# Kernel tuning notes

Measured on AMD Instinct MI355X. Metric: run time of the kernel, lower is better.

## Reference

```python
import jax, jax.numpy as jnp
import numpy as np

B, S, E, H = 4, 2048, 1024, 16
D = E // H  # head dim = 64

def setup_inputs() -> dict:
    key = jax.random.key(0)
    k1, k2, k3 = jax.random.split(key, 3)
    scale = 0.02
    return {
        "x": jax.random.normal(k1, (B, S, E), dtype=jnp.float32),
        "W_qkv": jax.random.normal(k2, (E, 3 * E), dtype=jnp.float32) * scale,
        "b_qkv": jnp.zeros((3 * E,), dtype=jnp.float32),
        "W_o": jax.random.normal(k3, (E, E), dtype=jnp.float32) * scale,
        "b_o": jnp.zeros((E,), dtype=jnp.float32),
    }

def reference(x, W_qkv, b_qkv, W_o, b_o):
    # dropout is identity in eval mode
    qkv = x @ W_qkv + b_qkv                      # [B, S, 3E]
    q, k, v = jnp.split(qkv, 3, axis=-1)          # each [B, S, E]
    def split_heads(t):
        return t.reshape(B, S, H, D).transpose(0, 2, 1, 3)  # [B, H, S, D]
    q, k, v = split_heads(q), split_heads(k), split_heads(v)
    scores = jnp.einsum("bhsd,bhtd->bhst", q, k) / jnp.sqrt(jnp.float32(D))
    causal = jnp.tril(jnp.ones((S, S), dtype=bool))
    scores = jnp.where(causal[None, None], scores, jnp.float32(-jnp.inf))
    attn = jax.nn.softmax(scores, axis=-1)        # [B, H, S, S]
    out = jnp.einsum("bhst,bhtd->bhsd", attn, v)  # [B, H, S, D]
    out = out.transpose(0, 2, 1, 3).reshape(B, S, E)
    return out @ W_o + b_o
```

## Files before the change

### kernel.cpp

```cpp
#include <hip/hip_runtime.h>
#include <stdint.h>

typedef __bf16 bf16_t;
typedef __bf16 bf16x8 __attribute__((ext_vector_type(8)));
typedef float f32x4 __attribute__((ext_vector_type(4)));

#define LOG2E 1.44269504088896340736f

__device__ __forceinline__ void gld_lds16(const bf16_t* g, bf16_t* l) {
    __builtin_amdgcn_global_load_lds(
        (__attribute__((address_space(1))) void*)(bf16_t*)g,
        (__attribute__((address_space(3))) void*)l,
        16, 0, 0);
}


__global__ void f32_to_bf16_k(const float* __restrict__ in, bf16_t* __restrict__ out) {
    int i = (blockIdx.x * 256 + threadIdx.x) * 4;
    float4 v = *(const float4*)(in + i);
    union { bf16_t b[4]; uint2 u; } u;
    u.b[0] = (bf16_t)v.x; u.b[1] = (bf16_t)v.y; u.b[2] = (bf16_t)v.z; u.b[3] = (bf16_t)v.w;
    *(uint2*)(out + i) = u.u;
}

__global__ void transpose_bf16_k(const float* __restrict__ in, bf16_t* __restrict__ out,
                                 int R, int C) {
    __shared__ float t[32][33];
    int tx = threadIdx.x, ty = threadIdx.y;
    int c0 = blockIdx.x * 32, r0 = blockIdx.y * 32;
    #pragma unroll
    for (int j = 0; j < 32; j += 8)
        t[ty + j][tx] = in[(size_t)(r0 + ty + j) * C + c0 + tx];
    __syncthreads();
    #pragma unroll
    for (int j = 0; j < 32; j += 8)
        out[(size_t)(c0 + ty + j) * R + r0 + tx] = (bf16_t)t[tx][ty + j];
}

__device__ __forceinline__ void gemm128_body(
    const bf16_t* __restrict__ A, const bf16_t* __restrict__ Bt,
    bf16_t* Al, bf16_t* Bl, f32x4 (&acc)[4][4], int m0, int n0, int Kd)
{
    const int tid = threadIdx.x;
    const int w = tid >> 6, lane = tid & 63;
    const int l15 = lane & 15, quad = lane >> 4;
    const int wm = w >> 1, wn = w & 1;

    const int scg = ((lane & 3) ^ ((lane >> 3) & 3)) * 8;
    const bf16_t* Ag = A + (size_t)(m0 + w * 32 + (lane >> 2)) * Kd + scg;
    const bf16_t* Bg = Bt + (size_t)(n0 + w * 32 + (lane >> 2)) * Kd + scg;
    bf16_t* Ald = Al + (w * 32) * 32;
    bf16_t* Bld = Bl + (w * 32) * 32;

    const int rc = (quad ^ ((l15 >> 1) & 3)) * 8;

    for (int k0 = 0; k0 < Kd; k0 += 32) {
        __syncthreads();
        gld_lds16(Ag + k0, Ald);
        gld_lds16(Ag + (size_t)16 * Kd + k0, Ald + 16 * 32);
        gld_lds16(Bg + k0, Bld);
        gld_lds16(Bg + (size_t)16 * Kd + k0, Bld + 16 * 32);
        __syncthreads();

        bf16x8 af[4], bf[4];
        #pragma unroll
        for (int mi = 0; mi < 4; mi++)
            af[mi] = *(const bf16x8*)(Al + (wm * 64 + mi * 16 + l15) * 32 + rc);
        #pragma unroll
        for (int ni = 0; ni < 4; ni++)
            bf[ni] = *(const bf16x8*)(Bl + (wn * 64 + ni * 16 + l15) * 32 + rc);
        #pragma unroll
        for (int mi = 0; mi < 4; mi++)
            #pragma unroll
            for (int ni = 0; ni < 4; ni++)
                acc[mi][ni] = __builtin_amdgcn_mfma_f32_16x16x32_bf16(
                    af[mi], bf[ni], acc[mi][ni], 0, 0, 0);
    }
}

__global__ __launch_bounds__(256) void gemm_qkv_k(
    const bf16_t* __restrict__ X, const bf16_t* __restrict__ WT,
    const float* __restrict__ bias,
    bf16_t* __restrict__ Qb, bf16_t* __restrict__ Kb, bf16_t* __restrict__ VTb)
{
    __shared__ bf16_t Al[128 * 32];
    __shared__ bf16_t Bl[128 * 32];
    const int tid = threadIdx.x;
    const int lane = tid & 63, w = tid >> 6;
    const int l15 = lane & 15, quad = lane >> 4;
    const int wm = w >> 1, wn = w & 1;
    const int m0 = blockIdx.y * 128, n0 = blockIdx.x * 128;

    f32x4 acc[4][4];
    #pragma unroll
    for (int mi = 0; mi < 4; mi++)
        #pragma unroll
        for (int ni = 0; ni < 4; ni++) acc[mi][ni] = (f32x4){0.f, 0.f, 0.f, 0.f};

    gemm128_body(X, WT, Al, Bl, acc, m0, n0, 1024);

    const float QSCALE = 0.125f * LOG2E;
    const int region = n0 >> 10;
    #pragma unroll
    for (int mi = 0; mi < 4; mi++) {
        const int mbase = m0 + wm * 64 + mi * 16 + quad * 4;
        const int b = mbase >> 11;
        const int sb = mbase & 2047;
        #pragma unroll
        for (int ni = 0; ni < 4; ni++) {
            const int n = n0 + wn * 64 + ni * 16 + l15;
            const float bia = bias[n];
            const int col = n & 1023;
            const int h = col >> 6, d = col & 63;
            if (region == 0) {
                bf16_t* dst = Qb + (((size_t)b * 16 + h) * 2048) * 64 + d;
                #pragma unroll
                for (int r = 0; r < 4; r++)
                    dst[(size_t)(sb + r) * 64] = (bf16_t)((acc[mi][ni][r] + bia) * QSCALE);
            } else if (region == 1) {
                bf16_t* dst = Kb + (((size_t)b * 16 + h) * 2048) * 64 + d;
                #pragma unroll
                for (int r = 0; r < 4; r++)
                    dst[(size_t)(sb + r) * 64] = (bf16_t)(acc[mi][ni][r] + bia);
            } else {
                union { bf16_t bv[4]; uint2 u; } u;
                #pragma unroll
                for (int r = 0; r < 4; r++) u.bv[r] = (bf16_t)(acc[mi][ni][r] + bia);
                *(uint2*)(VTb + (((size_t)b * 16 + h) * 64 + d) * 2048 + sb) = u.u;
            }
        }
    }
}

__global__ __launch_bounds__(256) void attn_k(
    const bf16_t* __restrict__ Qb, const bf16_t* __restrict__ Kb,
    const bf16_t* __restrict__ VTb, bf16_t* __restrict__ Ob)
{
    __shared__ bf16_t Kl[64 * 64];
    __shared__ bf16_t Vl[64 * 64];
    __shared__ bf16_t Pl[4][16 * 72];

    const int tid = threadIdx.x;
    const int w = tid >> 6, lane = tid & 63;
    const int l15 = lane & 15, quad = lane >> 4;
    const int idx = blockIdx.x;
    const int qt = 31 - (idx >> 6);
    const int bh = idx & 63;
    const int b = bh >> 4, h = bh & 15;
    const int q0 = qt * 64;

    const bf16_t* Qp = Qb + (size_t)bh * 2048 * 64;
    const bf16_t* Kp = Kb + (size_t)bh * 2048 * 64;
    const bf16_t* Vp = VTb + (size_t)bh * 64 * 2048;

    const int srow = w * 16 + (lane >> 3);
    const int scol = ((lane & 7) ^ ((lane >> 3) & 7)) * 8;
    const int rc0 = (quad ^ (l15 & 7)) * 8;
    const int rc1 = ((quad + 4) ^ (l15 & 7)) * 8;

    const int qrow = q0 + w * 16 + l15;
    bf16x8 aq0 = *(const bf16x8*)(Qp + (size_t)qrow * 64 + quad * 8);
    bf16x8 aq1 = *(const bf16x8*)(Qp + (size_t)qrow * 64 + 32 + quad * 8);

    bf16x8 vone;
    #pragma unroll
    for (int j = 0; j < 8; j++) vone[j] = (bf16_t)1.0f;

    f32x4 o[4];
    #pragma unroll
    for (int ni = 0; ni < 4; ni++) o[ni] = (f32x4){0.f, 0.f, 0.f, 0.f};
    f32x4 lacc = (f32x4){0.f, 0.f, 0.f, 0.f};

    for (int kv0 = 0; kv0 <= q0; kv0 += 64) {
        __syncthreads();
        gld_lds16(Kp + (size_t)(kv0 + srow) * 64 + scol, Kl + (w * 16) * 64);
        gld_lds16(Kp + (size_t)(kv0 + srow + 8) * 64 + scol, Kl + (w * 16 + 8) * 64);
        gld_lds16(Vp + (size_t)srow * 2048 + kv0 + scol, Vl + (w * 16) * 64);
        gld_lds16(Vp + (size_t)(srow + 8) * 2048 + kv0 + scol, Vl + (w * 16 + 8) * 64);
        __syncthreads();

        f32x4 sv[4];
        #pragma unroll
        for (int ni = 0; ni < 4; ni++) {
            bf16x8 bk0 = *(const bf16x8*)(Kl + (ni * 16 + l15) * 64 + rc0);
            bf16x8 bk1 = *(const bf16x8*)(Kl + (ni * 16 + l15) * 64 + rc1);
            f32x4 z = (f32x4){0.f, 0.f, 0.f, 0.f};
            z = __builtin_amdgcn_mfma_f32_16x16x32_bf16(aq0, bk0, z, 0, 0, 0);
            z = __builtin_amdgcn_mfma_f32_16x16x32_bf16(aq1, bk1, z, 0, 0, 0);
            sv[ni] = z;
        }

        if (kv0 == q0) {
            #pragma unroll
            for (int r = 0; r < 4; r++) {
                const int q = q0 + w * 16 + quad * 4 + r;
                #pragma unroll
                for (int ni = 0; ni < 4; ni++)
                    if (kv0 + ni * 16 + l15 > q) sv[ni][r] = -INFINITY;
            }
        }

        #pragma unroll
        for (int r = 0; r < 4; r++)
            #pragma unroll
            for (int ni = 0; ni < 4; ni++)
                Pl[w][(quad * 4 + r) * 72 + ni * 16 + l15] = (bf16_t)exp2f(sv[ni][r]);

        bf16x8 pa0 = *(const bf16x8*)(&Pl[w][l15 * 72 + quad * 8]);
        bf16x8 pa1 = *(const bf16x8*)(&Pl[w][l15 * 72 + 32 + quad * 8]);
        #pragma unroll
        for (int ni = 0; ni < 4; ni++) {
            bf16x8 bv0 = *(const bf16x8*)(Vl + (ni * 16 + l15) * 64 + rc0);
            bf16x8 bv1 = *(const bf16x8*)(Vl + (ni * 16 + l15) * 64 + rc1);
            o[ni] = __builtin_amdgcn_mfma_f32_16x16x32_bf16(pa0, bv0, o[ni], 0, 0, 0);
            o[ni] = __builtin_amdgcn_mfma_f32_16x16x32_bf16(pa1, bv1, o[ni], 0, 0, 0);
        }
        lacc = __builtin_amdgcn_mfma_f32_16x16x32_bf16(pa0, vone, lacc, 0, 0, 0);
        lacc = __builtin_amdgcn_mfma_f32_16x16x32_bf16(pa1, vone, lacc, 0, 0, 0);
    }

    #pragma unroll
    for (int r = 0; r < 4; r++) {
        const float inv = 1.0f / lacc[r];
        const int s = q0 + w * 16 + quad * 4 + r;
        #pragma unroll
        for (int ni = 0; ni < 4; ni++) {
            const int d = ni * 16 + l15;
            Ob[((size_t)b * 2048 + s) * 1024 + h * 64 + d] = (bf16_t)(o[ni][r] * inv);
        }
    }
}

__global__ __launch_bounds__(256) void gemm_out_k(
    const bf16_t* __restrict__ O, const bf16_t* __restrict__ WT,
    const float* __restrict__ bias, float* __restrict__ out)
{
    __shared__ bf16_t Al[128 * 32];
    __shared__ bf16_t Bl[128 * 32];
    const int tid = threadIdx.x;
    const int lane = tid & 63, w = tid >> 6;
    const int l15 = lane & 15, quad = lane >> 4;
    const int wm = w >> 1, wn = w & 1;
    const int m0 = blockIdx.y * 128, n0 = blockIdx.x * 128;

    f32x4 acc[4][4];
    #pragma unroll
    for (int mi = 0; mi < 4; mi++)
        #pragma unroll
        for (int ni = 0; ni < 4; ni++) acc[mi][ni] = (f32x4){0.f, 0.f, 0.f, 0.f};

    gemm128_body(O, WT, Al, Bl, acc, m0, n0, 1024);

    #pragma unroll
    for (int mi = 0; mi < 4; mi++) {
        const int mbase = m0 + wm * 64 + mi * 16 + quad * 4;
        #pragma unroll
        for (int ni = 0; ni < 4; ni++) {
            const int n = n0 + wn * 64 + ni * 16 + l15;
            const float bia = bias[n];
            #pragma unroll
            for (int r = 0; r < 4; r++)
                out[(size_t)(mbase + r) * 1024 + n] = acc[mi][ni][r] + bia;
        }
    }
}


extern "C" void kernel_launch(void* const* d_in, const int* in_sizes, int n_in,
                              void* d_out, int out_size, void* d_ws, size_t ws_size,
                              hipStream_t stream) {
    const float* x     = (const float*)d_in[0];
    const float* W_qkv = (const float*)d_in[1];
    const float* b_qkv = (const float*)d_in[2];
    const float* W_o   = (const float*)d_in[3];
    const float* b_o   = (const float*)d_in[4];
    float* out = (float*)d_out;

    char* ws = (char*)d_ws;
    size_t off = 0;
    auto alloc = [&](size_t bytes) -> void* {
        void* p = ws + off;
        off += (bytes + 255) & ~(size_t)255;
        return p;
    };
    bf16_t* xb    = (bf16_t*)alloc((size_t)8192 * 1024 * 2);
    bf16_t* wqkvT = (bf16_t*)alloc((size_t)3072 * 1024 * 2);
    bf16_t* woT   = (bf16_t*)alloc((size_t)1024 * 1024 * 2);
    bf16_t* Qb    = (bf16_t*)alloc((size_t)8192 * 1024 * 2);
    bf16_t* Kb    = (bf16_t*)alloc((size_t)8192 * 1024 * 2);
    bf16_t* VTb   = (bf16_t*)alloc((size_t)8192 * 1024 * 2);
    bf16_t* Ob    = xb;

    f32_to_bf16_k<<<8192, 256, 0, stream>>>(x, xb);
    transpose_bf16_k<<<dim3(96, 32), dim3(32, 8), 0, stream>>>(W_qkv, wqkvT, 1024, 3072);
    transpose_bf16_k<<<dim3(32, 32), dim3(32, 8), 0, stream>>>(W_o, woT, 1024, 1024);
    gemm_qkv_k<<<dim3(24, 64), 256, 0, stream>>>(xb, wqkvT, b_qkv, Qb, Kb, VTb);
    attn_k<<<2048, 256, 0, stream>>>(Qb, Kb, VTb, Ob);
    gemm_out_k<<<dim3(8, 64), 256, 0, stream>>>(Ob, woT, b_o, out);
}
```

Before: 261.8 us.

## Swap MFMA operand roles for vectorized epilogue stores and fuse prep kernels

Swaps the A/B operand order in the GEMMs and attention MFMAs so that each lane's four accumulator values lie along contiguous output elements. Q/K/O and the final fp32 output can then be written as packed 8- or 16-byte stores instead of strided scalar stores. The three preprocessing kernels are merged into one launch, and exp2 now uses the hardware builtin. The cost is that the V^T store becomes strided, and the grid order changes, which affects L2 reuse.

```diff
diff --git a/kernel.cpp b/kernel.cpp
--- a/kernel.cpp
+++ b/kernel.cpp
@@ -6,6 +6,14 @@
 typedef float f32x4 __attribute__((ext_vector_type(4)));
 
 #define LOG2E 1.44269504088896340736f
+
+__device__ __forceinline__ float fexp2(float x) {
+#if __has_builtin(__builtin_amdgcn_exp2f)
+    return __builtin_amdgcn_exp2f(x);
+#else
+    return exp2f(x);
+#endif
+}
 
 __device__ __forceinline__ void gld_lds16(const bf16_t* g, bf16_t* l) {
     __builtin_amdgcn_global_load_lds(
@@ -14,20 +22,28 @@
         16, 0, 0);
 }
 
-
-__global__ void f32_to_bf16_k(const float* __restrict__ in, bf16_t* __restrict__ out) {
-    int i = (blockIdx.x * 256 + threadIdx.x) * 4;
-    float4 v = *(const float4*)(in + i);
-    union { bf16_t b[4]; uint2 u; } u;
-    u.b[0] = (bf16_t)v.x; u.b[1] = (bf16_t)v.y; u.b[2] = (bf16_t)v.z; u.b[3] = (bf16_t)v.w;
-    *(uint2*)(out + i) = u.u;
-}
-
-__global__ void transpose_bf16_k(const float* __restrict__ in, bf16_t* __restrict__ out,
-                                 int R, int C) {
+__global__ __launch_bounds__(256) void prep_k(
+    const float* __restrict__ x, bf16_t* __restrict__ xb,
+    const float* __restrict__ Wqkv, bf16_t* __restrict__ wqkvT,
+    const float* __restrict__ Wo, bf16_t* __restrict__ woT)
+{
     __shared__ float t[32][33];
-    int tx = threadIdx.x, ty = threadIdx.y;
-    int c0 = blockIdx.x * 32, r0 = blockIdx.y * 32;
+    const int tid = threadIdx.x;
+    int blk = blockIdx.x;
+    if (blk < 8192) {
+        int i = blk * 1024 + tid * 4;
+        float4 v = *(const float4*)(x + i);
+        union { bf16_t b[4]; uint2 u; } u;
+        u.b[0] = (bf16_t)v.x; u.b[1] = (bf16_t)v.y; u.b[2] = (bf16_t)v.z; u.b[3] = (bf16_t)v.w;
+        *(uint2*)(xb + i) = u.u;
+        return;
+    }
+    const float* in; bf16_t* out; int C, bx, by;
+    if (blk < 11264) { blk -= 8192; in = Wqkv; out = wqkvT; C = 3072; bx = blk % 96; by = blk / 96; }
+    else             { blk -= 11264; in = Wo;   out = woT;   C = 1024; bx = blk % 32; by = blk / 32; }
+    const int R = 1024;
+    const int tx = tid & 31, ty = tid >> 5;
+    const int c0 = bx * 32, r0 = by * 32;
     #pragma unroll
     for (int j = 0; j < 32; j += 8)
         t[ty + j][tx] = in[(size_t)(r0 + ty + j) * C + c0 + tx];
@@ -89,7 +105,8 @@
     const int lane = tid & 63, w = tid >> 6;
     const int l15 = lane & 15, quad = lane >> 4;
     const int wm = w >> 1, wn = w & 1;
-    const int m0 = blockIdx.y * 128, n0 = blockIdx.x * 128;
+    const int n0 = blockIdx.x * 128;
+    const int m0 = blockIdx.y * 128;
 
     f32x4 acc[4][4];
     #pragma unroll
@@ -97,36 +114,38 @@
         #pragma unroll
         for (int ni = 0; ni < 4; ni++) acc[mi][ni] = (f32x4){0.f, 0.f, 0.f, 0.f};
 
-    gemm128_body(X, WT, Al, Bl, acc, m0, n0, 1024);
+    gemm128_body(WT, X, Al, Bl, acc, m0, n0, 1024);
 
     const float QSCALE = 0.125f * LOG2E;
-    const int region = n0 >> 10;
+    const int region = m0 >> 10;
     #pragma unroll
     for (int mi = 0; mi < 4; mi++) {
         const int mbase = m0 + wm * 64 + mi * 16 + quad * 4;
-        const int b = mbase >> 11;
-        const int sb = mbase & 2047;
+        const float4 bia = *(const float4*)(bias + mbase);
+        const float ba[4] = {bia.x, bia.y, bia.z, bia.w};
+        const int col = mbase & 1023;
+        const int h = col >> 6, dbase = col & 63;
         #pragma unroll
         for (int ni = 0; ni < 4; ni++) {
             const int n = n0 + wn * 64 + ni * 16 + l15;
-            const float bia = bias[n];
-            const int col = n & 1023;
-            const int h = col >> 6, d = col & 63;
+            const int b = n >> 11, s = n & 2047;
             if (region == 0) {
-                bf16_t* dst = Qb + (((size_t)b * 16 + h) * 2048) * 64 + d;
+                union { bf16_t bv[4]; uint2 u; } u;
                 #pragma unroll
                 for (int r = 0; r < 4; r++)
-                    dst[(size_t)(sb + r) * 64] = (bf16_t)((acc[mi][ni][r] + bia) * QSCALE);
+                    u.bv[r] = (bf16_t)((acc[mi][ni][r] + ba[r]) * QSCALE);
+                *(uint2*)(Qb + (((size_t)b * 16 + h) * 2048 + s) * 64 + dbase) = u.u;
             } else if (region == 1) {
-                bf16_t* dst = Kb + (((size_t)b * 16 + h) * 2048) * 64 + d;
+                union { bf16_t bv[4]; uint2 u; } u;
                 #pragma unroll
                 for (int r = 0; r < 4; r++)
-                    dst[(size_t)(sb + r) * 64] = (bf16_t)(acc[mi][ni][r] + bia);
+                    u.bv[r] = (bf16_t)(acc[mi][ni][r] + ba[r]);
+                *(uint2*)(Kb + (((size_t)b * 16 + h) * 2048 + s) * 64 + dbase) = u.u;
             } else {
-                union { bf16_t bv[4]; uint2 u; } u;
+                bf16_t* dst = VTb + (((size_t)b * 16 + h) * 64 + dbase) * 2048 + s;
                 #pragma unroll
-                for (int r = 0; r < 4; r++) u.bv[r] = (bf16_t)(acc[mi][ni][r] + bia);
-                *(uint2*)(VTb + (((size_t)b * 16 + h) * 64 + d) * 2048 + sb) = u.u;
+                for (int r = 0; r < 4; r++)
+                    dst[(size_t)r * 2048] = (bf16_t)(acc[mi][ni][r] + ba[r]);
             }
         }
     }
@@ -170,6 +189,7 @@
     #pragma unroll
     for (int ni = 0; ni < 4; ni++) o[ni] = (f32x4){0.f, 0.f, 0.f, 0.f};
     f32x4 lacc = (f32x4){0.f, 0.f, 0.f, 0.f};
+    const int qloc = w * 16 + l15;
 
     for (int kv0 = 0; kv0 <= q0; kv0 += 64) {
         __syncthreads();
@@ -182,29 +202,29 @@
         f32x4 sv[4];
         #pragma unroll
         for (int ni = 0; ni < 4; ni++) {
-            bf16x8 bk0 = *(const bf16x8*)(Kl + (ni * 16 + l15) * 64 + rc0);
-            bf16x8 bk1 = *(const bf16x8*)(Kl + (ni * 16 + l15) * 64 + rc1);
+            bf16x8 ak0 = *(const bf16x8*)(Kl + (ni * 16 + l15) * 64 + rc0);
+            bf16x8 ak1 = *(const bf16x8*)(Kl + (ni * 16 + l15) * 64 + rc1);
             f32x4 z = (f32x4){0.f, 0.f, 0.f, 0.f};
-            z = __builtin_amdgcn_mfma_f32_16x16x32_bf16(aq0, bk0, z, 0, 0, 0);
-            z = __builtin_amdgcn_mfma_f32_16x16x32_bf16(aq1, bk1, z, 0, 0, 0);
+            z = __builtin_amdgcn_mfma_f32_16x16x32_bf16(ak0, aq0, z, 0, 0, 0);
+            z = __builtin_amdgcn_mfma_f32_16x16x32_bf16(ak1, aq1, z, 0, 0, 0);
             sv[ni] = z;
         }
 
         if (kv0 == q0) {
             #pragma unroll
-            for (int r = 0; r < 4; r++) {
-                const int q = q0 + w * 16 + quad * 4 + r;
+            for (int ni = 0; ni < 4; ni++)
                 #pragma unroll
-                for (int ni = 0; ni < 4; ni++)
-                    if (kv0 + ni * 16 + l15 > q) sv[ni][r] = -INFINITY;
-            }
-        }
-
-        #pragma unroll
-        for (int r = 0; r < 4; r++)
+                for (int r = 0; r < 4; r++)
+                    if (ni * 16 + quad * 4 + r > qloc) sv[ni][r] = -INFINITY;
+        }
+
+        #pragma unroll
+        for (int ni = 0; ni < 4; ni++) {
+            union { bf16_t bv[4]; uint2 u; } pk;
             #pragma unroll
-            for (int ni = 0; ni < 4; ni++)
-                Pl[w][(quad * 4 + r) * 72 + ni * 16 + l15] = (bf16_t)exp2f(sv[ni][r]);
+            for (int r = 0; r < 4; r++) pk.bv[r] = (bf16_t)fexp2(sv[ni][r]);
+            *(uint2*)(&Pl[w][l15 * 72 + ni * 16 + quad * 4]) = pk.u;
+        }
 
         bf16x8 pa0 = *(const bf16x8*)(&Pl[w][l15 * 72 + quad * 8]);
         bf16x8 pa1 = *(const bf16x8*)(&Pl[w][l15 * 72 + 32 + quad * 8]);
@@ -212,22 +232,22 @@
         for (int ni = 0; ni < 4; ni++) {
             bf16x8 bv0 = *(const bf16x8*)(Vl + (ni * 16 + l15) * 64 + rc0);
             bf16x8 bv1 = *(const bf16x8*)(Vl + (ni * 16 + l15) * 64 + rc1);
-            o[ni] = __builtin_amdgcn_mfma_f32_16x16x32_bf16(pa0, bv0, o[ni], 0, 0, 0);
-            o[ni] = __builtin_amdgcn_mfma_f32_16x16x32_bf16(pa1, bv1, o[ni], 0, 0, 0);
-        }
-        lacc = __builtin_amdgcn_mfma_f32_16x16x32_bf16(pa0, vone, lacc, 0, 0, 0);
-        lacc = __builtin_amdgcn_mfma_f32_16x16x32_bf16(pa1, vone, lacc, 0, 0, 0);
-    }
-
-    #pragma unroll
-    for (int r = 0; r < 4; r++) {
-        const float inv = 1.0f / lacc[r];
-        const int s = q0 + w * 16 + quad * 4 + r;
-        #pragma unroll
-        for (int ni = 0; ni < 4; ni++) {
-            const int d = ni * 16 + l15;
-            Ob[((size_t)b * 2048 + s) * 1024 + h * 64 + d] = (bf16_t)(o[ni][r] * inv);
-        }
+            o[ni] = __builtin_amdgcn_mfma_f32_16x16x32_bf16(bv0, pa0, o[ni], 0, 0, 0);
+            o[ni] = __builtin_amdgcn_mfma_f32_16x16x32_bf16(bv1, pa1, o[ni], 0, 0, 0);
+        }
+        lacc = __builtin_amdgcn_mfma_f32_16x16x32_bf16(vone, pa0, lacc, 0, 0, 0);
+        lacc = __builtin_amdgcn_mfma_f32_16x16x32_bf16(vone, pa1, lacc, 0, 0, 0);
+    }
+
+    const float inv = 1.0f / lacc[0];
+    const int s = q0 + w * 16 + l15;
+    bf16_t* obase = Ob + ((size_t)b * 2048 + s) * 1024 + h * 64;
+    #pragma unroll
+    for (int ni = 0; ni < 4; ni++) {
+        union { bf16_t bv[4]; uint2 u; } u;
+        #pragma unroll
+        for (int r = 0; r < 4; r++) u.bv[r] = (bf16_t)(o[ni][r] * inv);
+        *(uint2*)(obase + ni * 16 + quad * 4) = u.u;
     }
 }
 
@@ -241,7 +261,8 @@
     const int lane = tid & 63, w = tid >> 6;
     const int l15 = lane & 15, quad = lane >> 4;
     const int wm = w >> 1, wn = w & 1;
-    const int m0 = blockIdx.y * 128, n0 = blockIdx.x * 128;
+    const int n0 = blockIdx.x * 128;
+    const int m0 = blockIdx.y * 128;
 
     f32x4 acc[4][4];
     #pragma unroll
@@ -249,18 +270,21 @@
         #pragma unroll
         for (int ni = 0; ni < 4; ni++) acc[mi][ni] = (f32x4){0.f, 0.f, 0.f, 0.f};
 
-    gemm128_body(O, WT, Al, Bl, acc, m0, n0, 1024);
+    gemm128_body(WT, O, Al, Bl, acc, m0, n0, 1024);
 
     #pragma unroll
     for (int mi = 0; mi < 4; mi++) {
         const int mbase = m0 + wm * 64 + mi * 16 + quad * 4;
+        const float4 bia = *(const float4*)(bias + mbase);
         #pragma unroll
         for (int ni = 0; ni < 4; ni++) {
             const int n = n0 + wn * 64 + ni * 16 + l15;
-            const float bia = bias[n];
-            #pragma unroll
-            for (int r = 0; r < 4; r++)
-                out[(size_t)(mbase + r) * 1024 + n] = acc[mi][ni][r] + bia;
+            float4 v;
+            v.x = acc[mi][ni][0] + bia.x;
+            v.y = acc[mi][ni][1] + bia.y;
+            v.z = acc[mi][ni][2] + bia.z;
+            v.w = acc[mi][ni][3] + bia.w;
+            *(float4*)(out + (size_t)n * 1024 + mbase) = v;
         }
     }
 }
@@ -291,10 +315,8 @@
     bf16_t* VTb   = (bf16_t*)alloc((size_t)8192 * 1024 * 2);
     bf16_t* Ob    = xb;
 
-    f32_to_bf16_k<<<8192, 256, 0, stream>>>(x, xb);
-    transpose_bf16_k<<<dim3(96, 32), dim3(32, 8), 0, stream>>>(W_qkv, wqkvT, 1024, 3072);
-    transpose_bf16_k<<<dim3(32, 32), dim3(32, 8), 0, stream>>>(W_o, woT, 1024, 1024);
-    gemm_qkv_k<<<dim3(24, 64), 256, 0, stream>>>(xb, wqkvT, b_qkv, Qb, Kb, VTb);
+    prep_k<<<12288, 256, 0, stream>>>(x, xb, W_qkv, wqkvT, W_o, woT);
+    gemm_qkv_k<<<dim3(64, 24), 256, 0, stream>>>(xb, wqkvT, b_qkv, Qb, Kb, VTb);
     attn_k<<<2048, 256, 0, stream>>>(Qb, Kb, VTb, Ob);
-    gemm_out_k<<<dim3(8, 64), 256, 0, stream>>>(Ob, woT, b_o, out);
-}
+    gemm_out_k<<<dim3(64, 8), 256, 0, stream>>>(Ob, woT, b_o, out);
+}
```

Result: faster. 253.0 us (-3.3%).
